# Performance work log

Measured on AMD Instinct MI355X. Metric: run time of the kernel, lower is better.

The kernel has to match this reference:

```python
import jax, jax.numpy as jnp
import numpy as np

B, S, D, H, HD, L, P = 32, 511, 512, 8, 64, 4, 501
PD = 32
FD = D - 2 * PD  # feature_proj output dim = hidden - 2*player_dim
DFF = 4 * D


def _pe(T, d):
    pos = jnp.arange(T, dtype=jnp.float32)[:, None]
    div = jnp.exp(jnp.arange(0, d, 2, dtype=jnp.float32) * (-np.log(10000.0) / d))
    pe = jnp.zeros((T, d), jnp.float32)
    pe = pe.at[:, 0::2].set(jnp.sin(pos * div))
    pe = pe.at[:, 1::2].set(jnp.cos(pos * div))
    return pe


def _ln(x, g, b, eps=1e-5):
    mu = x.mean(-1, keepdims=True)
    v = jnp.mean((x - mu) ** 2, -1, keepdims=True)
    return (x - mu) * jax.lax.rsqrt(v + eps) * g + b


def _forward(runs, wickets, overs, batters, bowlers, player_embed, Wf, bf,
             query_token, Wq, bq, Wk, bk, Wv, bv, Wo, bo,
             rec_s, bow_s, bat_s, W1, b1, W2, b2, g1, be1, g2, be2, Wout, bout):
    Bt, St = runs.shape
    T = St + 1
    # ball embedding: [B,S,3]@[3,FD] cat player embeds -> [B,S,D]
    feats = jnp.stack([runs, wickets, overs], -1) @ Wf + bf
    x = jnp.concatenate([feats, player_embed[batters], player_embed[bowlers]], -1)
    # append learned query token, add sinusoidal PE
    x = jnp.concatenate([x, jnp.broadcast_to(query_token, (Bt, 1, D))], 1)
    x = x + _pe(T, D)[None]
    # actor masks, padded with ones for the query row/col -> [B,T,T]
    sb = (bowlers[:, :, None] == bowlers[:, None, :]).astype(x.dtype)
    sm = (batters[:, :, None] == batters[:, None, :]).astype(x.dtype)
    row = jnp.ones((Bt, 1, St), x.dtype)
    col = jnp.ones((Bt, T, 1), x.dtype)
    sb = jnp.concatenate([jnp.concatenate([sb, row], 1), col], 2)
    sm = jnp.concatenate([jnp.concatenate([sm, row], 1), col], 2)
    causal = jnp.triu(jnp.ones((T, T), bool), 1)
    rec = jnp.arange(T, dtype=x.dtype) / T  # recency bias over key positions
    scale = 1.0 / np.float32(np.sqrt(HD))
    for l in range(L):
        q = (x @ Wq[l] + bq[l]).reshape(Bt, T, H, HD).transpose(0, 2, 1, 3)
        k = (x @ Wk[l] + bk[l]).reshape(Bt, T, H, HD).transpose(0, 2, 1, 3)
        v = (x @ Wv[l] + bv[l]).reshape(Bt, T, H, HD).transpose(0, 2, 1, 3)
        scores = jnp.einsum('bhqd,bhkd->bhqk', q, k) * scale
        # specialized head biases (num_heads >= 3)
        scores = scores.at[:, 0].add((rec_s[l] * rec)[None, None, :])
        scores = scores.at[:, 1].add(bow_s[l] * sb)
        scores = scores.at[:, 2].add(bat_s[l] * sm)
        scores = jnp.where(causal[None, None], -jnp.inf, scores)
        a = jax.nn.softmax(scores, axis=-1)
        o = jnp.einsum('bhqk,bhkd->bhqd', a, v).transpose(0, 2, 1, 3).reshape(Bt, T, D)
        x = _ln(x + o @ Wo[l] + bo[l], g1[l], be1[l])
        ff = jax.nn.gelu(x @ W1[l] + b1[l], approximate=False) @ W2[l] + b2[l]
        x = _ln(x + ff, g2[l], be2[l])
    return x[:, -1] @ Wout + bout  # [B, D]


def setup_inputs() -> dict:
    key = jax.random.key(0)
    ks = jax.random.split(key, 16)
    w = lambda k, sh: (0.02 * jax.random.normal(k, sh)).astype(jnp.float32)
    return {
        'runs': jax.random.uniform(ks[0], (B, S), jnp.float32),
        'wickets': jax.random.uniform(ks[1], (B, S), jnp.float32),
        'overs': jax.random.uniform(ks[2], (B, S), jnp.float32),
        'batters': jax.random.randint(ks[3], (B, S), 0, 500, jnp.int32),
        'bowlers': jax.random.randint(ks[4], (B, S), 0, 500, jnp.int32),
        'player_embed': w(ks[5], (P, PD)),
        'Wf': w(ks[6], (3, FD)), 'bf': jnp.zeros((FD,), jnp.float32),
        'query_token': jax.random.normal(ks[7], (1, 1, D), jnp.float32),
        'Wq': w(ks[8], (L, D, D)), 'bq': jnp.zeros((L, D), jnp.float32),
        'Wk': w(ks[9], (L, D, D)), 'bk': jnp.zeros((L, D), jnp.float32),
        'Wv': w(ks[10], (L, D, D)), 'bv': jnp.zeros((L, D), jnp.float32),
        'Wo': w(ks[11], (L, D, D)), 'bo': jnp.zeros((L, D), jnp.float32),
        'rec_s': jnp.full((L,), 0.5, jnp.float32),
        'bow_s': jnp.full((L,), 2.0, jnp.float32),
        'bat_s': jnp.full((L,), 2.0, jnp.float32),
        'W1': w(ks[12], (L, D, DFF)), 'b1': jnp.zeros((L, DFF), jnp.float32),
        'W2': w(ks[13], (L, DFF, D)), 'b2': jnp.zeros((L, D), jnp.float32),
        'g1': jnp.ones((L, D), jnp.float32), 'be1': jnp.zeros((L, D), jnp.float32),
        'g2': jnp.ones((L, D), jnp.float32), 'be2': jnp.zeros((L, D), jnp.float32),
        'Wout': w(ks[14], (D, D)), 'bout': jnp.zeros((D,), jnp.float32),
    }


def reference(runs, wickets, overs, batters, bowlers, player_embed, Wf, bf,
              query_token, Wq, bq, Wk, bk, Wv, bv, Wo, bo,
              rec_s, bow_s, bat_s, W1, b1, W2, b2, g1, be1, g2, be2, Wout, bout):
    return _forward(runs, wickets, overs, batters, bowlers, player_embed, Wf, bf,
                    query_token, Wq, bq, Wk, bk, Wv, bv, Wo, bo,
                    rec_s, bow_s, bat_s, W1, b1, W2, b2, g1, be1, g2, be2, Wout, bout)
```

## Files before the change

### kernel.cpp

```cpp
#include <hip/hip_runtime.h>
#include <math.h>

#define B_ 32
#define S_ 511
#define T_ 512
#define D_ 512
#define H_ 8
#define HD_ 64
#define L_ 4
#define P_ 501
#define PD_ 32
#define FD_ 448
#define DFF_ 2048

typedef __attribute__((ext_vector_type(8))) short bf16x8;
typedef __attribute__((ext_vector_type(4))) float f32x4;

#define GLDS16(gp, lp) __builtin_amdgcn_global_load_lds(                      \
    (const __attribute__((address_space(1))) void*)(gp),                      \
    (__attribute__((address_space(3))) void*)(lp), 16, 0, 0)

__device__ __forceinline__ unsigned short f2bf(float f) {
  union { float f; unsigned int u; } c; c.f = f;
  unsigned int r = c.u + 0x7FFFu + ((c.u >> 16) & 1u);
  return (unsigned short)(r >> 16);
}

__global__ __launch_bounds__(256) void wtrans_kernel(
    const float* __restrict__ in, unsigned short* __restrict__ out, int K, int N)
{
  __shared__ float t[64][65];
  const int l = blockIdx.z;
  in  += (size_t)l * K * N;
  out += (size_t)l * N * K;
  const int k0 = blockIdx.x * 64, n0 = blockIdx.y * 64;
  const int tx = threadIdx.x & 63, ty = threadIdx.x >> 6;
#pragma unroll
  for (int i = 0; i < 16; ++i) {
    int r = ty + i * 4;
    t[r][tx] = in[(size_t)(k0 + r) * N + n0 + tx];
  }
  __syncthreads();
#pragma unroll
  for (int i = 0; i < 16; ++i) {
    int r = ty + i * 4;
    out[(size_t)(n0 + r) * K + k0 + tx] = f2bf(t[tx][r]);
  }
}

__global__ __launch_bounds__(256) void embed_kernel(
    const float* __restrict__ runs, const float* __restrict__ wickets,
    const float* __restrict__ overs, const int* __restrict__ batters,
    const int* __restrict__ bowlers, const float* __restrict__ pemb,
    const float* __restrict__ Wf, const float* __restrict__ bfv,
    const float* __restrict__ qtok, float* __restrict__ x,
    unsigned short* __restrict__ xb)
{
  size_t idx = (size_t)blockIdx.x * 256 + threadIdx.x;
  const size_t total = (size_t)B_ * T_ * D_;
  if (idx >= total) return;
  int d = (int)(idx % D_);
  int t = (int)((idx / D_) % T_);
  int b = (int)(idx / ((size_t)D_ * T_));
  float val;
  if (t < S_) {
    size_t st = (size_t)b * S_ + t;
    if (d < FD_) {
      val = runs[st] * Wf[d] + wickets[st] * Wf[FD_ + d] + overs[st] * Wf[2 * FD_ + d] + bfv[d];
    } else if (d < FD_ + PD_) {
      val = pemb[(size_t)batters[st] * PD_ + (d - FD_)];
    } else {
      val = pemb[(size_t)bowlers[st] * PD_ + (d - FD_ - PD_)];
    }
  } else {
    val = qtok[d];
  }
  float div = expf((float)(2 * (d >> 1)) * (-9.210340371976184f / (float)D_));
  float ang = (float)t * div;
  val += (d & 1) ? cosf(ang) : sinf(ang);
  x[idx] = val;
  xb[idx] = f2bf(val);
}

template<int ACT>
__global__ __launch_bounds__(256) void mfma_gemm(
    const unsigned short* __restrict__ A, const unsigned short* __restrict__ Bt,
    const float* __restrict__ bias, float* __restrict__ C,
    unsigned short* __restrict__ Cb, int N, int K)
{
  __shared__ unsigned short As[2][128 * 32];
  __shared__ unsigned short Bs[2][128 * 32];
  __shared__ unsigned short Ts[ACT == 3 ? 128 * 136 : 1];
  const int tid = threadIdx.x;
  const int m0 = blockIdx.y * 128, n0 = blockIdx.x * 128;
  const int lane = tid & 63, w = tid >> 6;
  const int wr = w >> 1, wc = w & 1;
  const int lr = lane & 15, lg = lane >> 4;

  f32x4 acc[4][4] = {};

  const int srow = w * 16 + (lane >> 2);
  const int sc8 = (lane & 3) * 8;
  const unsigned short* gA0 = A + (size_t)(m0 + srow) * K + sc8;
  const unsigned short* gA1 = gA0 + (size_t)64 * K;
  const unsigned short* gB0 = Bt + (size_t)(n0 + srow) * K + sc8;
  const unsigned short* gB1 = gB0 + (size_t)64 * K;
  const int lofs0 = (w * 16) * 32;
  const int lofs1 = (64 + w * 16) * 32;

#define STAGE(buf, kk)                                                        \
  do {                                                                        \
    GLDS16(gA0 + (kk), &As[buf][lofs0]);                                      \
    GLDS16(gA1 + (kk), &As[buf][lofs1]);                                      \
    GLDS16(gB0 + (kk), &Bs[buf][lofs0]);                                      \
    GLDS16(gB1 + (kk), &Bs[buf][lofs1]);                                      \
  } while (0)

  STAGE(0, 0);
  __syncthreads();
  int cur = 0;
  for (int k0 = 0; k0 < K; k0 += 32) {
    if (k0 + 32 < K) STAGE(cur ^ 1, k0 + 32);
    bf16x8 af[4], bfr[4];
#pragma unroll
    for (int f = 0; f < 4; ++f) {
      af[f]  = *(const bf16x8*)&As[cur][(wr * 64 + f * 16 + lr) * 32 + lg * 8];
      bfr[f] = *(const bf16x8*)&Bs[cur][(wc * 64 + f * 16 + lr) * 32 + lg * 8];
    }
#pragma unroll
    for (int i = 0; i < 4; ++i)
#pragma unroll
      for (int j = 0; j < 4; ++j)
        acc[i][j] = __builtin_amdgcn_mfma_f32_16x16x32_bf16(af[i], bfr[j], acc[i][j], 0, 0, 0);
    __syncthreads();
    cur ^= 1;
  }
#undef STAGE

  const int crow0 = m0 + wr * 64 + lg * 4;
  const int ccol0 = n0 + wc * 64 + lr;
#pragma unroll
  for (int i = 0; i < 4; ++i) {
#pragma unroll
    for (int j = 0; j < 4; ++j) {
      const int col = ccol0 + j * 16;
      const float bcol = bias[col];
#pragma unroll
      for (int r = 0; r < 4; ++r) {
        const int row = crow0 + i * 16 + r;
        float v = acc[i][j][r] + bcol;
        if (ACT == 1) {
          v = 0.5f * v * (1.0f + erff(v * 0.70710678118654752f));
          Cb[(size_t)row * N + col] = f2bf(v);
        } else if (ACT == 2) {
          Cb[(size_t)row * N + col] = f2bf(v);
        } else if (ACT == 3) {
          Ts[(wc * 64 + j * 16 + lr) * 136 + (wr * 64 + i * 16 + lg * 4 + r)] = f2bf(v);
        } else {
          C[(size_t)row * N + col] = v;
        }
      }
    }
  }
  if (ACT == 3) {
    __syncthreads();
    const int c = tid & 127, h2 = tid >> 7;
    const int hh = (n0 + c) >> 6, hd = (n0 + c) & 63;
    const int bb = m0 >> 9, t0 = (m0 & (T_ - 1)) + h2 * 64;
    unsigned short* dst = Cb + (((size_t)bb * H_ + hh) * HD_ + hd) * T_ + t0;
#pragma unroll
    for (int e = 0; e < 8; ++e)
      *(bf16x8*)(dst + e * 8) = *(const bf16x8*)&Ts[c * 136 + h2 * 64 + e * 8];
  }
}

__global__ __launch_bounds__(256) void flash_mfma_kernel(
    const unsigned short* __restrict__ q, const unsigned short* __restrict__ k,
    const unsigned short* __restrict__ vt, unsigned short* __restrict__ o,
    const int* __restrict__ batters, const int* __restrict__ bowlers,
    const float* __restrict__ rec_sp, const float* __restrict__ bow_sp,
    const float* __restrict__ bat_sp, int l)
{
  __shared__ unsigned short QPs[64 * 70];
  __shared__ unsigned short Ks[64 * 70];
  __shared__ unsigned short Vs[64 * 70];
  __shared__ int aq_s[64], ak_s[64];

  const int p = blockIdx.x, h = blockIdx.y, b = blockIdx.z;
  const int tid = threadIdx.x;
  const int w = tid >> 6, lane = tid & 63;
  const int c = lane & 15, g = lane >> 4;
  const int NT = T_ / 64;

  int mode = 0; float hs = 0.f;
  if (h == 0) { mode = 1; hs = rec_sp[l]; }
  else if (h == 1) { mode = 2; hs = bow_sp[l]; }
  else if (h == 2) { mode = 3; hs = bat_sp[l]; }
  const int* actors = (mode == 2) ? bowlers : batters;

  const int sr = tid >> 2, sch = (tid & 3) * 16;

  for (int ph = 0; ph < 2; ++ph) {
    const int qt = (ph == 0) ? p : (NT - 1 - p);
    const int q0 = qt * 64;
    __syncthreads();

    {
      const unsigned short* src = q + ((size_t)b * T_ + q0 + sr) * D_ + h * HD_ + sch;
      *(bf16x8*)&QPs[sr * 70 + sch]     = *(const bf16x8*)src;
      *(bf16x8*)&QPs[sr * 70 + sch + 8] = *(const bf16x8*)(src + 8);
    }
    if (tid < 64) {
      int qg_ = q0 + tid;
      aq_s[tid] = (mode >= 2 && qg_ < S_) ? actors[(size_t)b * S_ + qg_] : -1;
    }
    __syncthreads();

    bf16x8 af0 = *(const bf16x8*)&QPs[(w * 16 + c) * 70 + g * 8];
    bf16x8 af1 = *(const bf16x8*)&QPs[(w * 16 + c) * 70 + 32 + g * 8];
    int aq4[4];
#pragma unroll
    for (int r = 0; r < 4; ++r) aq4[r] = aq_s[w * 16 + 4 * g + r];

    float m_r[4] = {-INFINITY, -INFINITY, -INFINITY, -INFINITY};
    float l_r[4] = {0.f, 0.f, 0.f, 0.f};
    f32x4 o_acc[4] = {};

    for (int kt = 0; kt <= qt; ++kt) {
      const int k0 = kt * 64;
      __syncthreads();
      {
        const unsigned short* ksrc = k + ((size_t)b * T_ + k0 + sr) * D_ + h * HD_ + sch;
        *(bf16x8*)&Ks[sr * 70 + sch]     = *(const bf16x8*)ksrc;
        *(bf16x8*)&Ks[sr * 70 + sch + 8] = *(const bf16x8*)(ksrc + 8);
        const unsigned short* vsrc = vt + ((size_t)(b * H_ + h) * HD_ + sr) * T_ + k0 + sch;
        *(bf16x8*)&Vs[sr * 70 + sch]     = *(const bf16x8*)vsrc;
        *(bf16x8*)&Vs[sr * 70 + sch + 8] = *(const bf16x8*)(vsrc + 8);
      }
      if (tid < 64) {
        int kg_ = k0 + tid;
        ak_s[tid] = (mode >= 2 && kg_ < S_) ? actors[(size_t)b * S_ + kg_] : -1;
      }
      __syncthreads();

      if (q0 + w * 16 + 15 < k0) continue;

      f32x4 s[4] = {};
#pragma unroll
      for (int f = 0; f < 4; ++f) {
        bf16x8 b0 = *(const bf16x8*)&Ks[(f * 16 + c) * 70 + g * 8];
        bf16x8 b1 = *(const bf16x8*)&Ks[(f * 16 + c) * 70 + 32 + g * 8];
        s[f] = __builtin_amdgcn_mfma_f32_16x16x32_bf16(af0, b0, s[f], 0, 0, 0);
        s[f] = __builtin_amdgcn_mfma_f32_16x16x32_bf16(af1, b1, s[f], 0, 0, 0);
      }

      int ak4[4];
#pragma unroll
      for (int f = 0; f < 4; ++f) ak4[f] = ak_s[f * 16 + c];

      float sv[4][4];
#pragma unroll
      for (int f = 0; f < 4; ++f) {
        const int kg = k0 + f * 16 + c;
#pragma unroll
        for (int r = 0; r < 4; ++r) {
          const int qg = q0 + w * 16 + 4 * g + r;
          float val = s[f][r] * 0.125f;
          if (mode == 1) {
            val = fmaf(hs, (float)kg * (1.0f / (float)T_), val);
          } else if (mode >= 2) {
            float eq = (qg == S_ || kg == S_) ? 1.0f : ((aq4[r] == ak4[f]) ? 1.0f : 0.0f);
            val = fmaf(hs, eq, val);
          }
          if (kg > qg) val = -INFINITY;
          sv[f][r] = val;
        }
      }
      float cr[4];
#pragma unroll
      for (int r = 0; r < 4; ++r) {
        float pm = fmaxf(fmaxf(sv[0][r], sv[1][r]), fmaxf(sv[2][r], sv[3][r]));
        pm = fmaxf(pm, __shfl_xor(pm, 1));
        pm = fmaxf(pm, __shfl_xor(pm, 2));
        pm = fmaxf(pm, __shfl_xor(pm, 4));
        pm = fmaxf(pm, __shfl_xor(pm, 8));
        float m_new = fmaxf(m_r[r], pm);
        cr[r] = __expf(m_r[r] - m_new);
        m_r[r] = m_new;
      }
      float rs[4] = {0.f, 0.f, 0.f, 0.f};
#pragma unroll
      for (int f = 0; f < 4; ++f) {
#pragma unroll
        for (int r = 0; r < 4; ++r) {
          float pv = __expf(sv[f][r] - m_r[r]);
          rs[r] += pv;
          QPs[(w * 16 + 4 * g + r) * 70 + f * 16 + c] = f2bf(pv);
        }
      }
#pragma unroll
      for (int r = 0; r < 4; ++r) {
        float t = rs[r];
        t += __shfl_xor(t, 1);
        t += __shfl_xor(t, 2);
        t += __shfl_xor(t, 4);
        t += __shfl_xor(t, 8);
        l_r[r] = l_r[r] * cr[r] + t;
#pragma unroll
        for (int f = 0; f < 4; ++f) o_acc[f][r] *= cr[r];
      }

      bf16x8 pa0 = *(const bf16x8*)&QPs[(w * 16 + c) * 70 + g * 8];
      bf16x8 pa1 = *(const bf16x8*)&QPs[(w * 16 + c) * 70 + 32 + g * 8];
#pragma unroll
      for (int f = 0; f < 4; ++f) {
        bf16x8 v0 = *(const bf16x8*)&Vs[(f * 16 + c) * 70 + g * 8];
        bf16x8 v1 = *(const bf16x8*)&Vs[(f * 16 + c) * 70 + 32 + g * 8];
        o_acc[f] = __builtin_amdgcn_mfma_f32_16x16x32_bf16(pa0, v0, o_acc[f], 0, 0, 0);
        o_acc[f] = __builtin_amdgcn_mfma_f32_16x16x32_bf16(pa1, v1, o_acc[f], 0, 0, 0);
      }
    }

#pragma unroll
    for (int r = 0; r < 4; ++r) {
      const float inv = 1.0f / l_r[r];
      const int row = q0 + w * 16 + 4 * g + r;
#pragma unroll
      for (int f = 0; f < 4; ++f)
        o[((size_t)b * T_ + row) * D_ + h * HD_ + f * 16 + c] = f2bf(o_acc[f][r] * inv);
    }
  }
}

__global__ __launch_bounds__(256) void add_ln_kernel(
    float* __restrict__ x, const float* __restrict__ y,
    const float* __restrict__ g, const float* __restrict__ be,
    unsigned short* __restrict__ xb)
{
  int row = blockIdx.x;
  int tid = threadIdx.x;
  size_t base = (size_t)row * D_;
  float v0 = x[base + tid] + y[base + tid];
  float v1 = x[base + tid + 256] + y[base + tid + 256];
  float s = v0 + v1;
  float s2 = v0 * v0 + v1 * v1;
  __shared__ float redA[4], redB[4];
#pragma unroll
  for (int off = 32; off > 0; off >>= 1) {
    s  += __shfl_down(s, off);
    s2 += __shfl_down(s2, off);
  }
  if ((tid & 63) == 0) { redA[tid >> 6] = s; redB[tid >> 6] = s2; }
  __syncthreads();
  float st  = redA[0] + redA[1] + redA[2] + redA[3];
  float s2t = redB[0] + redB[1] + redB[2] + redB[3];
  float mu = st * (1.0f / (float)D_);
  float var = s2t * (1.0f / (float)D_) - mu * mu;
  float r = rsqrtf(var + 1e-5f);
  float o0 = (v0 - mu) * r * g[tid] + be[tid];
  float o1 = (v1 - mu) * r * g[tid + 256] + be[tid + 256];
  x[base + tid]        = o0;
  x[base + tid + 256]  = o1;
  xb[base + tid]       = f2bf(o0);
  xb[base + tid + 256] = f2bf(o1);
}

__global__ __launch_bounds__(256) void final_kernel(
    const float* __restrict__ x, const float* __restrict__ Wout,
    const float* __restrict__ bout, float* __restrict__ out)
{
  __shared__ float xs[D_];
  int b = blockIdx.x;
  int n = blockIdx.y * 256 + threadIdx.x;
  const float* xr = x + ((size_t)b * T_ + (T_ - 1)) * D_;
  xs[threadIdx.x] = xr[threadIdx.x];
  xs[threadIdx.x + 256] = xr[threadIdx.x + 256];
  __syncthreads();
  float acc = bout[n];
  for (int kk = 0; kk < D_; ++kk)
    acc = fmaf(xs[kk], Wout[(size_t)kk * D_ + n], acc);
  out[(size_t)b * D_ + n] = acc;
}

extern "C" void kernel_launch(void* const* d_in, const int* in_sizes, int n_in,
                              void* d_out, int out_size, void* d_ws, size_t ws_size,
                              hipStream_t stream)
{
  const float* runs    = (const float*)d_in[0];
  const float* wickets = (const float*)d_in[1];
  const float* overs   = (const float*)d_in[2];
  const int*   batters = (const int*)d_in[3];
  const int*   bowlers = (const int*)d_in[4];
  const float* pemb    = (const float*)d_in[5];
  const float* Wf      = (const float*)d_in[6];
  const float* bfv     = (const float*)d_in[7];
  const float* qtok    = (const float*)d_in[8];
  const float* Wq      = (const float*)d_in[9];
  const float* bq      = (const float*)d_in[10];
  const float* Wk      = (const float*)d_in[11];
  const float* bk      = (const float*)d_in[12];
  const float* Wv      = (const float*)d_in[13];
  const float* bv      = (const float*)d_in[14];
  const float* Wo      = (const float*)d_in[15];
  const float* bo      = (const float*)d_in[16];
  const float* rec_s   = (const float*)d_in[17];
  const float* bow_s   = (const float*)d_in[18];
  const float* bat_s   = (const float*)d_in[19];
  const float* W1      = (const float*)d_in[20];
  const float* b1      = (const float*)d_in[21];
  const float* W2      = (const float*)d_in[22];
  const float* b2      = (const float*)d_in[23];
  const float* g1      = (const float*)d_in[24];
  const float* be1     = (const float*)d_in[25];
  const float* g2      = (const float*)d_in[26];
  const float* be2     = (const float*)d_in[27];
  const float* Wout    = (const float*)d_in[28];
  const float* bout    = (const float*)d_in[29];

  float* ws = (float*)d_ws;
  const size_t n1 = (size_t)B_ * T_ * D_;
  float* x  = ws;
  float* yb = ws + n1;
  unsigned short* xb   = (unsigned short*)(ws + 2 * n1);
  unsigned short* qb16 = xb + n1;
  unsigned short* kb16 = qb16 + n1;
  unsigned short* vb16 = kb16 + n1;
  unsigned short* vt   = vb16 + n1;
  unsigned short* ob   = vt + n1;
  unsigned short* wt   = ob + n1;
  unsigned short* hb   = qb16;

  const size_t wsz = (size_t)L_ * D_ * D_;
  unsigned short* wtq = wt;
  unsigned short* wtk = wtq + wsz;
  unsigned short* wtv = wtk + wsz;
  unsigned short* wto = wtv + wsz;
  unsigned short* wt1 = wto + wsz;
  unsigned short* wt2 = wt1 + (size_t)L_ * D_ * DFF_;

  const int M = B_ * T_;
  dim3 blk(256);

  wtrans_kernel<<<dim3(8, 8, L_),  blk, 0, stream>>>(Wq, wtq, D_, D_);
  wtrans_kernel<<<dim3(8, 8, L_),  blk, 0, stream>>>(Wk, wtk, D_, D_);
  wtrans_kernel<<<dim3(8, 8, L_),  blk, 0, stream>>>(Wv, wtv, D_, D_);
  wtrans_kernel<<<dim3(8, 8, L_),  blk, 0, stream>>>(Wo, wto, D_, D_);
  wtrans_kernel<<<dim3(8, 32, L_), blk, 0, stream>>>(W1, wt1, D_, DFF_);
  wtrans_kernel<<<dim3(32, 8, L_), blk, 0, stream>>>(W2, wt2, DFF_, D_);

  {
    size_t total = (size_t)B_ * T_ * D_;
    int nb = (int)((total + 255) / 256);
    embed_kernel<<<nb, blk, 0, stream>>>(runs, wickets, overs, batters, bowlers,
                                         pemb, Wf, bfv, qtok, x, xb);
  }

  for (int l = 0; l < L_; ++l) {
    mfma_gemm<2><<<dim3(D_ / 128, M / 128), blk, 0, stream>>>(
        xb, wtq + (size_t)l * D_ * D_, bq + l * D_, nullptr, qb16, D_, D_);
    mfma_gemm<2><<<dim3(D_ / 128, M / 128), blk, 0, stream>>>(
        xb, wtk + (size_t)l * D_ * D_, bk + l * D_, nullptr, kb16, D_, D_);
    mfma_gemm<3><<<dim3(D_ / 128, M / 128), blk, 0, stream>>>(
        xb, wtv + (size_t)l * D_ * D_, bv + l * D_, nullptr, vt, D_, D_);

    flash_mfma_kernel<<<dim3(T_ / 128, H_, B_), blk, 0, stream>>>(
        qb16, kb16, vt, ob, batters, bowlers, rec_s, bow_s, bat_s, l);

    mfma_gemm<0><<<dim3(D_ / 128, M / 128), blk, 0, stream>>>(
        ob, wto + (size_t)l * D_ * D_, bo + l * D_, yb, nullptr, D_, D_);
    add_ln_kernel<<<M, blk, 0, stream>>>(x, yb, g1 + l * D_, be1 + l * D_, xb);

    mfma_gemm<1><<<dim3(DFF_ / 128, M / 128), blk, 0, stream>>>(
        xb, wt1 + (size_t)l * D_ * DFF_, b1 + l * DFF_, nullptr, hb, DFF_, D_);
    mfma_gemm<0><<<dim3(D_ / 128, M / 128), blk, 0, stream>>>(
        hb, wt2 + (size_t)l * DFF_ * D_, b2 + l * D_, yb, nullptr, D_, DFF_);
    add_ln_kernel<<<M, blk, 0, stream>>>(x, yb, g2 + l * D_, be2 + l * D_, xb);
  }

  final_kernel<<<dim3(B_, D_ / 256), blk, 0, stream>>>(x, Wout, bout, (float*)d_out);
}
```

Before: 1.399 ms.

## Fuse Q/K projections into one GEMM and double-buffer K/V tiles in flash attention

Q and K weights are packed into one 1024-wide transposed matrix, so a single GEMM with a split bias produces an interleaved QK buffer. That removes one launch and one extra read of the activations per layer. The flash attention kernel now double-buffers K/V tiles in shared memory, loading the next tile into registers while computing on the current one, and drops one barrier per iteration. The cost is more shared memory per block and higher register pressure, which may lower occupancy.

Measured after the change: 1.349 ms. -3.6%, faster.

```diff
diff --git a/kernel.cpp b/kernel.cpp
--- a/kernel.cpp
+++ b/kernel.cpp
@@ -27,12 +27,13 @@
 }
 
 __global__ __launch_bounds__(256) void wtrans_kernel(
-    const float* __restrict__ in, unsigned short* __restrict__ out, int K, int N)
+    const float* __restrict__ in, unsigned short* __restrict__ out, int K, int N,
+    size_t lstride, int nofs)
 {
   __shared__ float t[64][65];
   const int l = blockIdx.z;
   in  += (size_t)l * K * N;
-  out += (size_t)l * N * K;
+  out += (size_t)l * lstride + (size_t)nofs * K;
   const int k0 = blockIdx.x * 64, n0 = blockIdx.y * 64;
   const int tx = threadIdx.x & 63, ty = threadIdx.x >> 6;
 #pragma unroll
@@ -86,7 +87,7 @@
 __global__ __launch_bounds__(256) void mfma_gemm(
     const unsigned short* __restrict__ A, const unsigned short* __restrict__ Bt,
     const float* __restrict__ bias, float* __restrict__ C,
-    unsigned short* __restrict__ Cb, int N, int K)
+    unsigned short* __restrict__ Cb, int N, int K, const float* __restrict__ bias2)
 {
   __shared__ unsigned short As[2][128 * 32];
   __shared__ unsigned short Bs[2][128 * 32];
@@ -144,7 +145,8 @@
 #pragma unroll
     for (int j = 0; j < 4; ++j) {
       const int col = ccol0 + j * 16;
-      const float bcol = bias[col];
+      const float bcol = (ACT == 4) ? ((col < 512) ? bias[col] : bias2[col - 512])
+                                    : bias[col];
 #pragma unroll
       for (int r = 0; r < 4; ++r) {
         const int row = crow0 + i * 16 + r;
@@ -152,7 +154,7 @@
         if (ACT == 1) {
           v = 0.5f * v * (1.0f + erff(v * 0.70710678118654752f));
           Cb[(size_t)row * N + col] = f2bf(v);
-        } else if (ACT == 2) {
+        } else if (ACT == 2 || ACT == 4) {
           Cb[(size_t)row * N + col] = f2bf(v);
         } else if (ACT == 3) {
           Ts[(wc * 64 + j * 16 + lr) * 136 + (wr * 64 + i * 16 + lg * 4 + r)] = f2bf(v);
@@ -175,16 +177,16 @@
 }
 
 __global__ __launch_bounds__(256) void flash_mfma_kernel(
-    const unsigned short* __restrict__ q, const unsigned short* __restrict__ k,
-    const unsigned short* __restrict__ vt, unsigned short* __restrict__ o,
+    const unsigned short* __restrict__ qk, const unsigned short* __restrict__ vt,
+    unsigned short* __restrict__ o,
     const int* __restrict__ batters, const int* __restrict__ bowlers,
     const float* __restrict__ rec_sp, const float* __restrict__ bow_sp,
     const float* __restrict__ bat_sp, int l)
 {
   __shared__ unsigned short QPs[64 * 70];
-  __shared__ unsigned short Ks[64 * 70];
-  __shared__ unsigned short Vs[64 * 70];
-  __shared__ int aq_s[64], ak_s[64];
+  __shared__ unsigned short Ks[2][64 * 70];
+  __shared__ unsigned short Vs[2][64 * 70];
+  __shared__ int aq_s[64], ak_s[2][64];
 
   const int p = blockIdx.x, h = blockIdx.y, b = blockIdx.z;
   const int tid = threadIdx.x;
@@ -199,6 +201,9 @@
   const int* actors = (mode == 2) ? bowlers : batters;
 
   const int sr = tid >> 2, sch = (tid & 3) * 16;
+  const unsigned short* qbase = qk + (size_t)b * T_ * 1024 + h * HD_;
+  const unsigned short* kbase = qbase + 512;
+  const unsigned short* vbase = vt + ((size_t)(b * H_ + h) * HD_ + sr) * T_;
 
   for (int ph = 0; ph < 2; ++ph) {
     const int qt = (ph == 0) ? p : (NT - 1 - p);
@@ -206,13 +211,20 @@
     __syncthreads();
 
     {
-      const unsigned short* src = q + ((size_t)b * T_ + q0 + sr) * D_ + h * HD_ + sch;
+      const unsigned short* src = qbase + (size_t)(q0 + sr) * 1024 + sch;
       *(bf16x8*)&QPs[sr * 70 + sch]     = *(const bf16x8*)src;
       *(bf16x8*)&QPs[sr * 70 + sch + 8] = *(const bf16x8*)(src + 8);
+      const unsigned short* ksrc = kbase + (size_t)sr * 1024 + sch;
+      *(bf16x8*)&Ks[0][sr * 70 + sch]     = *(const bf16x8*)ksrc;
+      *(bf16x8*)&Ks[0][sr * 70 + sch + 8] = *(const bf16x8*)(ksrc + 8);
+      const unsigned short* vsrc = vbase + sch;
+      *(bf16x8*)&Vs[0][sr * 70 + sch]     = *(const bf16x8*)vsrc;
+      *(bf16x8*)&Vs[0][sr * 70 + sch + 8] = *(const bf16x8*)(vsrc + 8);
     }
     if (tid < 64) {
       int qg_ = q0 + tid;
       aq_s[tid] = (mode >= 2 && qg_ < S_) ? actors[(size_t)b * S_ + qg_] : -1;
+      ak_s[0][tid] = (mode >= 2 && tid < S_) ? actors[(size_t)b * S_ + tid] : -1;
     }
     __syncthreads();
 
@@ -225,99 +237,110 @@
     float m_r[4] = {-INFINITY, -INFINITY, -INFINITY, -INFINITY};
     float l_r[4] = {0.f, 0.f, 0.f, 0.f};
     f32x4 o_acc[4] = {};
+    int cur = 0;
 
     for (int kt = 0; kt <= qt; ++kt) {
       const int k0 = kt * 64;
-      __syncthreads();
-      {
-        const unsigned short* ksrc = k + ((size_t)b * T_ + k0 + sr) * D_ + h * HD_ + sch;
-        *(bf16x8*)&Ks[sr * 70 + sch]     = *(const bf16x8*)ksrc;
-        *(bf16x8*)&Ks[sr * 70 + sch + 8] = *(const bf16x8*)(ksrc + 8);
-        const unsigned short* vsrc = vt + ((size_t)(b * H_ + h) * HD_ + sr) * T_ + k0 + sch;
-        *(bf16x8*)&Vs[sr * 70 + sch]     = *(const bf16x8*)vsrc;
-        *(bf16x8*)&Vs[sr * 70 + sch + 8] = *(const bf16x8*)(vsrc + 8);
+      const bool has_next = kt < qt;
+      bf16x8 kr0, kr1, vr0, vr1;
+      int akn = -1;
+      if (has_next) {
+        const int k0n = k0 + 64;
+        const unsigned short* ksrc = kbase + (size_t)(k0n + sr) * 1024 + sch;
+        kr0 = *(const bf16x8*)ksrc;
+        kr1 = *(const bf16x8*)(ksrc + 8);
+        const unsigned short* vsrc = vbase + k0n + sch;
+        vr0 = *(const bf16x8*)vsrc;
+        vr1 = *(const bf16x8*)(vsrc + 8);
+        if (tid < 64) {
+          int kg_ = k0n + tid;
+          akn = (mode >= 2 && kg_ < S_) ? actors[(size_t)b * S_ + kg_] : -1;
+        }
       }
-      if (tid < 64) {
-        int kg_ = k0 + tid;
-        ak_s[tid] = (mode >= 2 && kg_ < S_) ? actors[(size_t)b * S_ + kg_] : -1;
+
+      if (q0 + w * 16 + 15 >= k0) {
+        f32x4 s[4] = {};
+#pragma unroll
+        for (int f = 0; f < 4; ++f) {
+          bf16x8 b0 = *(const bf16x8*)&Ks[cur][(f * 16 + c) * 70 + g * 8];
+          bf16x8 b1 = *(const bf16x8*)&Ks[cur][(f * 16 + c) * 70 + 32 + g * 8];
+          s[f] = __builtin_amdgcn_mfma_f32_16x16x32_bf16(af0, b0, s[f], 0, 0, 0);
+          s[f] = __builtin_amdgcn_mfma_f32_16x16x32_bf16(af1, b1, s[f], 0, 0, 0);
+        }
+        int ak4[4];
+#pragma unroll
+        for (int f = 0; f < 4; ++f) ak4[f] = ak_s[cur][f * 16 + c];
+
+        float sv[4][4];
+#pragma unroll
+        for (int f = 0; f < 4; ++f) {
+          const int kg = k0 + f * 16 + c;
+#pragma unroll
+          for (int r = 0; r < 4; ++r) {
+            const int qg = q0 + w * 16 + 4 * g + r;
+            float val = s[f][r] * 0.125f;
+            if (mode == 1) {
+              val = fmaf(hs, (float)kg * (1.0f / (float)T_), val);
+            } else if (mode >= 2) {
+              float eq = (qg == S_ || kg == S_) ? 1.0f : ((aq4[r] == ak4[f]) ? 1.0f : 0.0f);
+              val = fmaf(hs, eq, val);
+            }
+            if (kg > qg) val = -INFINITY;
+            sv[f][r] = val;
+          }
+        }
+        float cr[4];
+#pragma unroll
+        for (int r = 0; r < 4; ++r) {
+          float pm = fmaxf(fmaxf(sv[0][r], sv[1][r]), fmaxf(sv[2][r], sv[3][r]));
+          pm = fmaxf(pm, __shfl_xor(pm, 1));
+          pm = fmaxf(pm, __shfl_xor(pm, 2));
+          pm = fmaxf(pm, __shfl_xor(pm, 4));
+          pm = fmaxf(pm, __shfl_xor(pm, 8));
+          float m_new = fmaxf(m_r[r], pm);
+          cr[r] = __expf(m_r[r] - m_new);
+          m_r[r] = m_new;
+        }
+        float rs[4] = {0.f, 0.f, 0.f, 0.f};
+#pragma unroll
+        for (int f = 0; f < 4; ++f) {
+#pragma unroll
+          for (int r = 0; r < 4; ++r) {
+            float pv = __expf(sv[f][r] - m_r[r]);
+            rs[r] += pv;
+            QPs[(w * 16 + 4 * g + r) * 70 + f * 16 + c] = f2bf(pv);
+          }
+        }
+#pragma unroll
+        for (int r = 0; r < 4; ++r) {
+          float t = rs[r];
+          t += __shfl_xor(t, 1);
+          t += __shfl_xor(t, 2);
+          t += __shfl_xor(t, 4);
+          t += __shfl_xor(t, 8);
+          l_r[r] = l_r[r] * cr[r] + t;
+#pragma unroll
+          for (int f = 0; f < 4; ++f) o_acc[f][r] *= cr[r];
+        }
+        bf16x8 pa0 = *(const bf16x8*)&QPs[(w * 16 + c) * 70 + g * 8];
+        bf16x8 pa1 = *(const bf16x8*)&QPs[(w * 16 + c) * 70 + 32 + g * 8];
+#pragma unroll
+        for (int f = 0; f < 4; ++f) {
+          bf16x8 v0 = *(const bf16x8*)&Vs[cur][(f * 16 + c) * 70 + g * 8];
+          bf16x8 v1 = *(const bf16x8*)&Vs[cur][(f * 16 + c) * 70 + 32 + g * 8];
+          o_acc[f] = __builtin_amdgcn_mfma_f32_16x16x32_bf16(pa0, v0, o_acc[f], 0, 0, 0);
+          o_acc[f] = __builtin_amdgcn_mfma_f32_16x16x32_bf16(pa1, v1, o_acc[f], 0, 0, 0);
+        }
       }
-      __syncthreads();
-
-      if (q0 + w * 16 + 15 < k0) continue;
-
-      f32x4 s[4] = {};
-#pragma unroll
-      for (int f = 0; f < 4; ++f) {
-        bf16x8 b0 = *(const bf16x8*)&Ks[(f * 16 + c) * 70 + g * 8];
-        bf16x8 b1 = *(const bf16x8*)&Ks[(f * 16 + c) * 70 + 32 + g * 8];
-        s[f] = __builtin_amdgcn_mfma_f32_16x16x32_bf16(af0, b0, s[f], 0, 0, 0);
-        s[f] = __builtin_amdgcn_mfma_f32_16x16x32_bf16(af1, b1, s[f], 0, 0, 0);
-      }
-
-      int ak4[4];
-#pragma unroll
-      for (int f = 0; f < 4; ++f) ak4[f] = ak_s[f * 16 + c];
-
-      float sv[4][4];
-#pragma unroll
-      for (int f = 0; f < 4; ++f) {
-        const int kg = k0 + f * 16 + c;
-#pragma unroll
-        for (int r = 0; r < 4; ++r) {
-          const int qg = q0 + w * 16 + 4 * g + r;
-          float val = s[f][r] * 0.125f;
-          if (mode == 1) {
-            val = fmaf(hs, (float)kg * (1.0f / (float)T_), val);
-          } else if (mode >= 2) {
-            float eq = (qg == S_ || kg == S_) ? 1.0f : ((aq4[r] == ak4[f]) ? 1.0f : 0.0f);
-            val = fmaf(hs, eq, val);
-          }
-          if (kg > qg) val = -INFINITY;
-          sv[f][r] = val;
-        }
-      }
-      float cr[4];
-#pragma unroll
-      for (int r = 0; r < 4; ++r) {
-        float pm = fmaxf(fmaxf(sv[0][r], sv[1][r]), fmaxf(sv[2][r], sv[3][r]));
-        pm = fmaxf(pm, __shfl_xor(pm, 1));
-        pm = fmaxf(pm, __shfl_xor(pm, 2));
-        pm = fmaxf(pm, __shfl_xor(pm, 4));
-        pm = fmaxf(pm, __shfl_xor(pm, 8));
-        float m_new = fmaxf(m_r[r], pm);
-        cr[r] = __expf(m_r[r] - m_new);
-        m_r[r] = m_new;
-      }
-      float rs[4] = {0.f, 0.f, 0.f, 0.f};
-#pragma unroll
-      for (int f = 0; f < 4; ++f) {
-#pragma unroll
-        for (int r = 0; r < 4; ++r) {
-          float pv = __expf(sv[f][r] - m_r[r]);
-          rs[r] += pv;
-          QPs[(w * 16 + 4 * g + r) * 70 + f * 16 + c] = f2bf(pv);
-        }
-      }
-#pragma unroll
-      for (int r = 0; r < 4; ++r) {
-        float t = rs[r];
-        t += __shfl_xor(t, 1);
-        t += __shfl_xor(t, 2);
-        t += __shfl_xor(t, 4);
-        t += __shfl_xor(t, 8);
-        l_r[r] = l_r[r] * cr[r] + t;
-#pragma unroll
-        for (int f = 0; f < 4; ++f) o_acc[f][r] *= cr[r];
-      }
-
-      bf16x8 pa0 = *(const bf16x8*)&QPs[(w * 16 + c) * 70 + g * 8];
-      bf16x8 pa1 = *(const bf16x8*)&QPs[(w * 16 + c) * 70 + 32 + g * 8];
-#pragma unroll
-      for (int f = 0; f < 4; ++f) {
-        bf16x8 v0 = *(const bf16x8*)&Vs[(f * 16 + c) * 70 + g * 8];
-        bf16x8 v1 = *(const bf16x8*)&Vs[(f * 16 + c) * 70 + 32 + g * 8];
-        o_acc[f] = __builtin_amdgcn_mfma_f32_16x16x32_bf16(pa0, v0, o_acc[f], 0, 0, 0);
-        o_acc[f] = __builtin_amdgcn_mfma_f32_16x16x32_bf16(pa1, v1, o_acc[f], 0, 0, 0);
+
+      if (has_next) {
+        *(bf16x8*)&Ks[cur ^ 1][sr * 70 + sch]     = kr0;
+        *(bf16x8*)&Ks[cur ^ 1][sr * 70 + sch + 8] = kr1;
+        *(bf16x8*)&Vs[cur ^ 1][sr * 70 + sch]     = vr0;
+        *(bf16x8*)&Vs[cur ^ 1][sr * 70 + sch + 8] = vr1;
+        if (tid < 64) ak_s[cur ^ 1][tid] = akn;
+        __syncthreads();
+        cur ^= 1;
       }
     }
 
@@ -421,32 +444,29 @@
   const size_t n1 = (size_t)B_ * T_ * D_;
   float* x  = ws;
   float* yb = ws + n1;
-  unsigned short* xb   = (unsigned short*)(ws + 2 * n1);
-  unsigned short* qb16 = xb + n1;
-  unsigned short* kb16 = qb16 + n1;
-  unsigned short* vb16 = kb16 + n1;
-  unsigned short* vt   = vb16 + n1;
-  unsigned short* ob   = vt + n1;
-  unsigned short* wt   = ob + n1;
-  unsigned short* hb   = qb16;
-
-  const size_t wsz = (size_t)L_ * D_ * D_;
-  unsigned short* wtq = wt;
-  unsigned short* wtk = wtq + wsz;
-  unsigned short* wtv = wtk + wsz;
-  unsigned short* wto = wtv + wsz;
-  unsigned short* wt1 = wto + wsz;
+  unsigned short* xb = (unsigned short*)(ws + 2 * n1);
+  unsigned short* qkb = xb + n1;
+  unsigned short* vt  = qkb + 2 * n1;
+  unsigned short* ob  = vt + n1;
+  unsigned short* wt  = ob + n1;
+  unsigned short* hb  = qkb;
+
+  const size_t qk_lstride = (size_t)1024 * 512;
+  unsigned short* wqk = wt;
+  unsigned short* wtv = wqk + (size_t)L_ * qk_lstride;
+  unsigned short* wto = wtv + (size_t)L_ * D_ * D_;
+  unsigned short* wt1 = wto + (size_t)L_ * D_ * D_;
   unsigned short* wt2 = wt1 + (size_t)L_ * D_ * DFF_;
 
   const int M = B_ * T_;
   dim3 blk(256);
 
-  wtrans_kernel<<<dim3(8, 8, L_),  blk, 0, stream>>>(Wq, wtq, D_, D_);
-  wtrans_kernel<<<dim3(8, 8, L_),  blk, 0, stream>>>(Wk, wtk, D_, D_);
-  wtrans_kernel<<<dim3(8, 8, L_),  blk, 0, stream>>>(Wv, wtv, D_, D_);
-  wtrans_kernel<<<dim3(8, 8, L_),  blk, 0, stream>>>(Wo, wto, D_, D_);
-  wtrans_kernel<<<dim3(8, 32, L_), blk, 0, stream>>>(W1, wt1, D_, DFF_);
-  wtrans_kernel<<<dim3(32, 8, L_), blk, 0, stream>>>(W2, wt2, DFF_, D_);
+  wtrans_kernel<<<dim3(8, 8, L_),  blk, 0, stream>>>(Wq, wqk, D_, D_, qk_lstride, 0);
+  wtrans_kernel<<<dim3(8, 8, L_),  blk, 0, stream>>>(Wk, wqk, D_, D_, qk_lstride, 512);
+  wtrans_kernel<<<dim3(8, 8, L_),  blk, 0, stream>>>(Wv, wtv, D_, D_, (size_t)D_ * D_, 0);
+  wtrans_kernel<<<dim3(8, 8, L_),  blk, 0, stream>>>(Wo, wto, D_, D_, (size_t)D_ * D_, 0);
+  wtrans_kernel<<<dim3(8, 32, L_), blk, 0, stream>>>(W1, wt1, D_, DFF_, (size_t)D_ * DFF_, 0);
+  wtrans_kernel<<<dim3(32, 8, L_), blk, 0, stream>>>(W2, wt2, DFF_, D_, (size_t)DFF_ * D_, 0);
 
   {
     size_t total = (size_t)B_ * T_ * D_;
@@ -456,24 +476,23 @@
   }
 
   for (int l = 0; l < L_; ++l) {
-    mfma_gemm<2><<<dim3(D_ / 128, M / 128), blk, 0, stream>>>(
-        xb, wtq + (size_t)l * D_ * D_, bq + l * D_, nullptr, qb16, D_, D_);
-    mfma_gemm<2><<<dim3(D_ / 128, M / 128), blk, 0, stream>>>(
-        xb, wtk + (size_t)l * D_ * D_, bk + l * D_, nullptr, kb16, D_, D_);
+    mfma_gemm<4><<<dim3(1024 / 128, M / 128), blk, 0, stream>>>(
+        xb, wqk + (size_t)l * qk_lstride, bq + l * D_, nullptr, qkb, 1024, D_,
+        bk + l * D_);
     mfma_gemm<3><<<dim3(D_ / 128, M / 128), blk, 0, stream>>>(
-        xb, wtv + (size_t)l * D_ * D_, bv + l * D_, nullptr, vt, D_, D_);
+        xb, wtv + (size_t)l * D_ * D_, bv + l * D_, nullptr, vt, D_, D_, nullptr);
 
     flash_mfma_kernel<<<dim3(T_ / 128, H_, B_), blk, 0, stream>>>(
-        qb16, kb16, vt, ob, batters, bowlers, rec_s, bow_s, bat_s, l);
+        qkb, vt, ob, batters, bowlers, rec_s, bow_s, bat_s, l);
 
     mfma_gemm<0><<<dim3(D_ / 128, M / 128), blk, 0, stream>>>(
-        ob, wto + (size_t)l * D_ * D_, bo + l * D_, yb, nullptr, D_, D_);
+        ob, wto + (size_t)l * D_ * D_, bo + l * D_, yb, nullptr, D_, D_, nullptr);
     add_ln_kernel<<<M, blk, 0, stream>>>(x, yb, g1 + l * D_, be1 + l * D_, xb);
 
     mfma_gemm<1><<<dim3(DFF_ / 128, M / 128), blk, 0, stream>>>(
-        xb, wt1 + (size_t)l * D_ * DFF_, b1 + l * DFF_, nullptr, hb, DFF_, D_);
+        xb, wt1 + (size_t)l * D_ * DFF_, b1 + l * DFF_, nullptr, hb, DFF_, D_, nullptr);
     mfma_gemm<0><<<dim3(D_ / 128, M / 128), blk, 0, stream>>>(
-        hb, wt2 + (size_t)l * DFF_ * D_, b2 + l * D_, yb, nullptr, D_, DFF_);
+        hb, wt2 + (size_t)l * DFF_ * D_, b2 + l * D_, yb, nullptr, D_, DFF_, nullptr);
     add_ln_kernel<<<M, blk, 0, stream>>>(x, yb, g2 + l * D_, be2 + l * D_, xb);
   }
 
```
